# Kernel optimization log

Measured on AMD Instinct MI355X. Metric: run time of the kernel, lower is better.

The kernel has to match this reference:

```python
import jax, jax.numpy as jnp
import numpy as np

N, E = 50000, 800000
F_IN, HID, HEADS, OUT = 128, 32, 4, 16
NEG_SLOPE = 0.2  # PyG GATConv default leaky_relu slope


def segment_softmax(logits, seg, n):
    # numerically stable softmax over edges grouped by destination node
    m = jax.ops.segment_max(logits, seg, num_segments=n)          # [N,H]
    m = jnp.where(jnp.isfinite(m), m, 0.0)                        # guard empty segments
    e = jnp.exp(logits - m[seg])                                  # [E,H]
    s = jax.ops.segment_sum(e, seg, num_segments=n)               # [N,H]
    return e / (s[seg] + 1e-16)


def gat_conv(x, W, a_src, a_dst, bias, src, dst, concat):
    H, C = a_src.shape
    n = x.shape[0]
    h = (x @ W).reshape(n, H, C)                                  # [N,H,C]
    alpha_src = jnp.einsum('nhc,hc->nh', h, a_src)                # [N,H]
    alpha_dst = jnp.einsum('nhc,hc->nh', h, a_dst)                # [N,H]
    e = jax.nn.leaky_relu(alpha_src[src] + alpha_dst[dst], NEG_SLOPE)  # [E,H]
    alpha = segment_softmax(e, dst, n)                            # [E,H]
    msg = h[src] * alpha[:, :, None]                              # [E,H,C]
    out = jax.ops.segment_sum(msg, dst, num_segments=n)           # [N,H,C]
    out = out.reshape(n, H * C) if concat else out.mean(axis=1)
    return out + bias


def setup_inputs() -> dict:
    key = jax.random.key(0)
    ks = jax.random.split(key, 12)
    s = 0.1  # keep attention logits in a sane range
    return {
        'x': jax.random.normal(ks[0], (N, F_IN), jnp.float32),
        'edge_index': jax.random.randint(ks[1], (2, E), 0, N),
        'Wemb': jax.random.normal(ks[2], (F_IN, HID), jnp.float32) * s,
        'bemb': jnp.zeros((HID,), jnp.float32),
        'W1': jax.random.normal(ks[3], (HID, HEADS * HID), jnp.float32) * s,
        'a_src1': jax.random.normal(ks[4], (HEADS, HID), jnp.float32) * s,
        'a_dst1': jax.random.normal(ks[5], (HEADS, HID), jnp.float32) * s,
        'b1': jnp.zeros((HEADS * HID,), jnp.float32),
        'W2': jax.random.normal(ks[6], (HEADS * HID, HEADS * OUT), jnp.float32) * s,
        'a_src2': jax.random.normal(ks[7], (HEADS, OUT), jnp.float32) * s,
        'a_dst2': jax.random.normal(ks[8], (HEADS, OUT), jnp.float32) * s,
        'b2': jnp.zeros((OUT,), jnp.float32),
    }


def reference(x, edge_index, Wemb, bemb, W1, a_src1, a_dst1, b1, W2, a_src2, a_dst2, b2):
    src, dst = edge_index[0], edge_index[1]
    h = x @ Wemb + bemb  # dropout layers are identity at inference
    h = jax.nn.elu(gat_conv(h, W1, a_src1, a_dst1, b1, src, dst, True))
    h = gat_conv(h, W2, a_src2, a_dst2, b2, src, dst, False)
    return jax.nn.log_softmax(h, axis=1)
```

## Files before the change

### kernel.cpp

```cpp
#include <hip/hip_runtime.h>

#define N_NODES 50000
#define N_EDGES 800000
#define F_IN    128
#define HID     32
#define HEADS   4
#define OUT_C   16

#define NBKT 196
#define CAP  5120
#define EPB  4096
#define NB64 782

typedef __attribute__((ext_vector_type(8))) short bf16x8;
typedef __attribute__((ext_vector_type(4))) float f32x4;

__device__ __forceinline__ unsigned short f2bf(float f) {
    unsigned int u = __float_as_uint(f);
    u += 0x7FFFu + ((u >> 16) & 1u);
    return (unsigned short)(u >> 16);
}
__device__ __forceinline__ float bf_lo(unsigned int u) { return __uint_as_float(u << 16); }
__device__ __forceinline__ float bf_hi(unsigned int u) { return __uint_as_float(u & 0xFFFF0000u); }
__device__ __forceinline__ float bf2f(unsigned short s) {
    return __uint_as_float(((unsigned int)s) << 16);
}

__device__ __forceinline__ float edge_w(float asv, float adv) {
    float v = asv + adv;
    v = (v > 0.f) ? v : 0.2f * v;
    return __expf(v);
}

__global__ __launch_bounds__(256) void k_F1(const float* __restrict__ x,
                                            const float* __restrict__ Wemb,
                                            const float* __restrict__ bemb,
                                            float* __restrict__ h0,
                                            unsigned short* __restrict__ h0b,
                                            const int* __restrict__ ei,
                                            int* __restrict__ gcnt,
                                            unsigned int* __restrict__ pairs) {
    __shared__ float xs[64][132];
    __shared__ float Wl[F_IN][HID];
    __shared__ float bl[HID];
    __shared__ int hist[NBKT];
    __shared__ int base[NBKT];
    int t = threadIdx.x;
    if (blockIdx.x < NB64) {
        int node0 = blockIdx.x * 64;
        if (t < HID) bl[t] = bemb[t];
        #pragma unroll
        for (int it = 0; it < 4; it++) {
            int idx = it * 256 + t;
            *(float4*)((float*)Wl + idx * 4) = *(const float4*)(Wemb + idx * 4);
        }
        #pragma unroll
        for (int it = 0; it < 8; it++) {
            int idx = it * 256 + t;
            int row = idx >> 5, c4 = idx & 31;
            float4 v = make_float4(0.f, 0.f, 0.f, 0.f);
            if (node0 + row < N_NODES) v = *(const float4*)(x + (size_t)(node0 + row) * F_IN + c4 * 4);
            *(float4*)&xs[row][c4 * 4] = v;
        }
        __syncthreads();
        int c = t & 7, g = t >> 3;
        float acc[2][4] = {};
        for (int k = 0; k < F_IN; k++) {
            float4 w4 = *(const float4*)&Wl[k][c * 4];
            #pragma unroll
            for (int n = 0; n < 2; n++) {
                float xv = xs[g * 2 + n][k];
                acc[n][0] += xv * w4.x; acc[n][1] += xv * w4.y;
                acc[n][2] += xv * w4.z; acc[n][3] += xv * w4.w;
            }
        }
        #pragma unroll
        for (int n = 0; n < 2; n++) {
            int node = node0 + g * 2 + n;
            if (node < N_NODES) {
                float4 o = make_float4(acc[n][0] + bl[c * 4], acc[n][1] + bl[c * 4 + 1],
                                       acc[n][2] + bl[c * 4 + 2], acc[n][3] + bl[c * 4 + 3]);
                *(float4*)(h0 + (size_t)node * HID + c * 4) = o;
                ushort4 ob;
                ob.x = f2bf(o.x); ob.y = f2bf(o.y); ob.z = f2bf(o.z); ob.w = f2bf(o.w);
                *(ushort4*)(h0b + (size_t)node * HID + c * 4) = ob;
            }
        }
    } else {
        int e0 = (blockIdx.x - NB64) * EPB;
        for (int i = t; i < NBKT; i += 256) hist[i] = 0;
        __syncthreads();
        unsigned int p[16];
        int bb[16];
        #pragma unroll
        for (int i = 0; i < 16; i++) {
            int e = e0 + i * 256 + t;
            bb[i] = -1;
            if (e < N_EDGES) {
                int s = ei[e], d = ei[N_EDGES + e];
                p[i] = ((unsigned int)s << 8) | (unsigned int)(d & 255);
                bb[i] = d >> 8;
                atomicAdd(&hist[bb[i]], 1);
            }
        }
        __syncthreads();
        for (int i = t; i < NBKT; i += 256) {
            int c = hist[i];
            base[i] = i * CAP + (c ? atomicAdd(&gcnt[i], c) : 0);
            hist[i] = 0;
        }
        __syncthreads();
        #pragma unroll
        for (int i = 0; i < 16; i++) {
            if (bb[i] >= 0) {
                int off = atomicAdd(&hist[bb[i]], 1);
                pairs[base[bb[i]] + off] = p[i];
            }
        }
    }
}

__global__ __launch_bounds__(256) void k_F2(const float* __restrict__ h0,
                                            const float* __restrict__ W1,
                                            const float* __restrict__ a_src,
                                            const float* __restrict__ a_dst,
                                            float* __restrict__ as, float* __restrict__ ad,
                                            const unsigned int* __restrict__ pairs,
                                            const int* __restrict__ gcnt,
                                            int* __restrict__ rowptr,
                                            int* __restrict__ esrc) {
    __shared__ float xs[64][36];
    __shared__ float Wl[HID][128];
    __shared__ int cnt[256];
    __shared__ int cur[256];
    __shared__ int wsum[4];
    int t = threadIdx.x;
    if (blockIdx.x < NB64) {
        int node0 = blockIdx.x * 64;
        #pragma unroll
        for (int it = 0; it < 4; it++) {
            int idx = it * 256 + t;
            *(float4*)((float*)Wl + idx * 4) = *(const float4*)(W1 + idx * 4);
        }
        #pragma unroll
        for (int it = 0; it < 2; it++) {
            int idx = it * 256 + t;
            int row = idx >> 3, c4 = idx & 7;
            float4 v = make_float4(0.f, 0.f, 0.f, 0.f);
            if (node0 + row < N_NODES) v = *(const float4*)(h0 + (size_t)(node0 + row) * HID + c4 * 4);
            *(float4*)&xs[row][c4 * 4] = v;
        }
        __syncthreads();
        int c = t & 31, g = t >> 5;
        float acc[8][4] = {};
        for (int k = 0; k < HID; k++) {
            float4 w4 = *(const float4*)&Wl[k][c * 4];
            #pragma unroll
            for (int n = 0; n < 8; n++) {
                float xv = xs[g * 8 + n][k];
                acc[n][0] += xv * w4.x; acc[n][1] += xv * w4.y;
                acc[n][2] += xv * w4.z; acc[n][3] += xv * w4.w;
            }
        }
        float4 av = *(const float4*)(a_src + c * 4);
        float4 dv = *(const float4*)(a_dst + c * 4);
        float ps[8], pd[8];
        #pragma unroll
        for (int n = 0; n < 8; n++) {
            ps[n] = acc[n][0] * av.x + acc[n][1] * av.y + acc[n][2] * av.z + acc[n][3] * av.w;
            pd[n] = acc[n][0] * dv.x + acc[n][1] * dv.y + acc[n][2] * dv.z + acc[n][3] * dv.w;
        }
        #pragma unroll
        for (int mask = 1; mask <= 4; mask <<= 1) {
            #pragma unroll
            for (int n = 0; n < 8; n++) {
                ps[n] += __shfl_xor(ps[n], mask, 64);
                pd[n] += __shfl_xor(pd[n], mask, 64);
            }
        }
        if ((c & 7) == 0) {
            int hh = c >> 3;
            #pragma unroll
            for (int n = 0; n < 8; n++) {
                int node = node0 + g * 8 + n;
                if (node < N_NODES) { as[node * 4 + hh] = ps[n]; ad[node * 4 + hh] = pd[n]; }
            }
        }
    } else {
        int b = blockIdx.x - NB64;
        int lane = t & 63, wv = t >> 6;
        int v0 = (t < NBKT && t < b) ? gcnt[t] : 0;
        #pragma unroll
        for (int mask = 1; mask < 64; mask <<= 1) v0 += __shfl_xor(v0, mask, 64);
        if (lane == 0) wsum[wv] = v0;
        __syncthreads();
        int base = wsum[0] + wsum[1] + wsum[2] + wsum[3];
        int n0 = b << 8;
        int cntb = gcnt[b];
        int s0 = b * CAP;
        cnt[t] = 0;
        __syncthreads();
        for (int i = t; i < cntb; i += 256) atomicAdd(&cnt[pairs[s0 + i] & 255], 1);
        __syncthreads();
        int v = cnt[t], x = v;
        #pragma unroll
        for (int off = 1; off < 64; off <<= 1) { int y = __shfl_up(x, off, 64); if (lane >= off) x += y; }
        __syncthreads();
        if (lane == 63) wsum[wv] = x;
        __syncthreads();
        int add = 0;
        for (int j = 0; j < wv; j++) add += wsum[j];
        int excl = base + (x - v) + add;
        cur[t] = excl;
        if (n0 + t < N_NODES) rowptr[n0 + t] = excl;
        if (b == 0 && t == 0) rowptr[N_NODES] = N_EDGES;
        __syncthreads();
        for (int i = t; i < cntb; i += 256) {
            unsigned int p = pairs[s0 + i];
            int pos = atomicAdd(&cur[p & 255], 1);
            esrc[pos] = (int)(p >> 8);
        }
    }
}

__global__ __launch_bounds__(256) void k_h2f(const unsigned int* __restrict__ hin,
                                             const float* __restrict__ W2,
                                             const float* __restrict__ a_src,
                                             const float* __restrict__ a_dst,
                                             unsigned short* __restrict__ h2,
                                             float* __restrict__ as, float* __restrict__ ad) {
    __shared__ unsigned int xsu[64][68];
    __shared__ unsigned short w2t[64][136];
    int t = threadIdx.x;
    int node0 = blockIdx.x * 64;
    #pragma unroll
    for (int it = 0; it < 4; it++) {
        int idx = it * 256 + t;
        int row = idx >> 4, c4 = idx & 15;
        uint4 v = make_uint4(0u, 0u, 0u, 0u);
        if (node0 + row < N_NODES) v = *(const uint4*)(hin + (size_t)(node0 + row) * 64 + c4 * 4);
        *(uint4*)&xsu[row][c4 * 4] = v;
    }
    #pragma unroll
    for (int it = 0; it < 8; it++) {
        int idx = it * 256 + t;
        int k = idx >> 4, n4 = idx & 15;
        float4 w = *(const float4*)(W2 + k * 64 + n4 * 4);
        w2t[n4 * 4 + 0][k] = f2bf(w.x);
        w2t[n4 * 4 + 1][k] = f2bf(w.y);
        w2t[n4 * 4 + 2][k] = f2bf(w.z);
        w2t[n4 * 4 + 3][k] = f2bf(w.w);
    }
    __syncthreads();
    int lane = t & 63, wv = t >> 6;
    int lrow = lane & 15, lk = lane >> 4;
    f32x4 acc[4] = {};
    const char* xbase = (const char*)&xsu[wv * 16 + lrow][0] + lk * 16;
    #pragma unroll
    for (int kt = 0; kt < 4; kt++) {
        bf16x8 af = *(const bf16x8*)(xbase + kt * 64);
        #pragma unroll
        for (int h = 0; h < 4; h++) {
            bf16x8 bfr = *(const bf16x8*)((const char*)&w2t[h * 16 + lrow][0] + kt * 64 + lk * 16);
            acc[h] = __builtin_amdgcn_mfma_f32_16x16x32_bf16(af, bfr, acc[h], 0, 0, 0);
        }
    }
    float av[4], dv[4];
    #pragma unroll
    for (int h = 0; h < 4; h++) { av[h] = a_src[h * 16 + lrow]; dv[h] = a_dst[h * 16 + lrow]; }
    #pragma unroll
    for (int r = 0; r < 4; r++) {
        int node = node0 + wv * 16 + lk * 4 + r;
        float psh[4], pdh[4];
        #pragma unroll
        for (int h = 0; h < 4; h++) {
            float v = acc[h][r];
            if (node < N_NODES) h2[(size_t)node * 64 + h * 16 + lrow] = f2bf(v);
            float p = v * av[h], q = v * dv[h];
            #pragma unroll
            for (int mask = 1; mask < 16; mask <<= 1) {
                p += __shfl_xor(p, mask, 64);
                q += __shfl_xor(q, mask, 64);
            }
            psh[h] = p; pdh[h] = q;
        }
        if (lrow == 0 && node < N_NODES) {
            *(float4*)(as + node * 4) = make_float4(psh[0], psh[1], psh[2], psh[3]);
            *(float4*)(ad + node * 4) = make_float4(pdh[0], pdh[1], pdh[2], pdh[3]);
        }
    }
}

__global__ __launch_bounds__(256) void k_gather1(const int* __restrict__ esrc,
                                                 const int* __restrict__ rowptr,
                                                 const unsigned int* __restrict__ h0b,
                                                 const float* __restrict__ as,
                                                 const float* __restrict__ ad,
                                                 const float* __restrict__ W1,
                                                 const float* __restrict__ b1,
                                                 unsigned int* __restrict__ out1) {
    __shared__ float Wl[HID][128];
    __shared__ float aw[4][4][32];
    int t = threadIdx.x;
    #pragma unroll
    for (int it = 0; it < 4; it++) {
        int idx = it * 256 + t;
        *(float4*)((float*)Wl + idx * 4) = *(const float4*)(W1 + idx * 4);
    }
    int node = blockIdx.x * 4 + (t >> 6);
    int lane = t & 63;
    int head = lane >> 4;
    int cp = lane & 15;
    int s16 = lane >> 2;
    int h4 = lane & 3;
    int lb = cp * 4;
    int hb = head * 4;
    int beg = rowptr[node], end = rowptr[node + 1];
    float ad_w = ad[node * 4 + h4];
    float ax = 0.f, ay = 0.f, s = 0.f;
    const char* hc = (const char*)h0b;
    for (int k = beg; k < end; k += 16) {
        int idx = k + s16;
        int sm = esrc[min(idx, end - 1)];
#define G1L(J) int sj##J = __builtin_amdgcn_readlane(sm, (J) * 4); \
        unsigned int u##J = *(const unsigned int*)(hc + (size_t)(unsigned)sj##J * 64 + lb);
        G1L(0)  G1L(1)  G1L(2)  G1L(3)  G1L(4)  G1L(5)  G1L(6)  G1L(7)
        G1L(8)  G1L(9)  G1L(10) G1L(11) G1L(12) G1L(13) G1L(14) G1L(15)
#undef G1L
        float wm = edge_w(as[sm * 4 + h4], ad_w);
        if (idx >= end) wm = 0.f;
        int wmi = __float_as_int(wm);
#define G1W(J) float w##J = __int_as_float(__builtin_amdgcn_ds_bpermute(hb + (J) * 16, wmi));
        G1W(0)  G1W(1)  G1W(2)  G1W(3)  G1W(4)  G1W(5)  G1W(6)  G1W(7)
        G1W(8)  G1W(9)  G1W(10) G1W(11) G1W(12) G1W(13) G1W(14) G1W(15)
#undef G1W
        ax += bf_lo(u0)  * w0  + bf_lo(u1)  * w1  + bf_lo(u2)  * w2  + bf_lo(u3)  * w3
            + bf_lo(u4)  * w4  + bf_lo(u5)  * w5  + bf_lo(u6)  * w6  + bf_lo(u7)  * w7
            + bf_lo(u8)  * w8  + bf_lo(u9)  * w9  + bf_lo(u10) * w10 + bf_lo(u11) * w11
            + bf_lo(u12) * w12 + bf_lo(u13) * w13 + bf_lo(u14) * w14 + bf_lo(u15) * w15;
        ay += bf_hi(u0)  * w0  + bf_hi(u1)  * w1  + bf_hi(u2)  * w2  + bf_hi(u3)  * w3
            + bf_hi(u4)  * w4  + bf_hi(u5)  * w5  + bf_hi(u6)  * w6  + bf_hi(u7)  * w7
            + bf_hi(u8)  * w8  + bf_hi(u9)  * w9  + bf_hi(u10) * w10 + bf_hi(u11) * w11
            + bf_hi(u12) * w12 + bf_hi(u13) * w13 + bf_hi(u14) * w14 + bf_hi(u15) * w15;
        s += (w0 + w1 + w2 + w3) + (w4 + w5 + w6 + w7)
           + (w8 + w9 + w10 + w11) + (w12 + w13 + w14 + w15);
    }
    float rs = 1.0f / (s + 1e-16f);
    int wv = t >> 6;
    aw[wv][head][cp * 2]     = ax * rs;
    aw[wv][head][cp * 2 + 1] = ay * rs;
    __syncthreads();
    float2 bv = *(const float2*)(b1 + 2 * lane);
    float vx = 0.f, vy = 0.f;
    #pragma unroll
    for (int k2 = 0; k2 < HID; k2++) {
        float a = aw[wv][head][k2];
        float2 w2 = *(const float2*)&Wl[k2][2 * lane];
        vx += a * w2.x; vy += a * w2.y;
    }
    vx += bv.x; vy += bv.y;
    vx = (vx > 0.f) ? vx : (__expf(vx) - 1.0f);
    vy = (vy > 0.f) ? vy : (__expf(vy) - 1.0f);
    out1[(size_t)node * 64 + lane] = ((unsigned int)f2bf(vy) << 16) | (unsigned int)f2bf(vx);
}

__global__ __launch_bounds__(256) void k_gather2(const int* __restrict__ esrc,
                                                 const int* __restrict__ rowptr,
                                                 const unsigned short* __restrict__ h2,
                                                 const float* __restrict__ as,
                                                 const float* __restrict__ ad,
                                                 const float* __restrict__ b2,
                                                 float* __restrict__ out) {
    int t = threadIdx.x;
    int node = blockIdx.x * 4 + (t >> 6);
    int lane = t & 63;
    int head = lane >> 4, c = lane & 15;
    int s16 = lane >> 2;
    int h4 = lane & 3;
    int lb = lane * 2;
    int hb = head * 4;
    int beg = rowptr[node], end = rowptr[node + 1];
    float ad_w = ad[node * 4 + h4];
    float acc = 0.f, s = 0.f;
    const char* h2c = (const char*)h2;
    for (int k = beg; k < end; k += 16) {
        int idx = k + s16;
        int sm = esrc[min(idx, end - 1)];
#define G2L(J) int sj##J = __builtin_amdgcn_readlane(sm, (J) * 4); \
        float r##J = bf2f(*(const unsigned short*)(h2c + (size_t)(unsigned)sj##J * 128 + lb));
        G2L(0)  G2L(1)  G2L(2)  G2L(3)  G2L(4)  G2L(5)  G2L(6)  G2L(7)
        G2L(8)  G2L(9)  G2L(10) G2L(11) G2L(12) G2L(13) G2L(14) G2L(15)
#undef G2L
        float wm = edge_w(as[sm * 4 + h4], ad_w);
        if (idx >= end) wm = 0.f;
        int wmi = __float_as_int(wm);
#define G2W(J) float w##J = __int_as_float(__builtin_amdgcn_ds_bpermute(hb + (J) * 16, wmi));
        G2W(0)  G2W(1)  G2W(2)  G2W(3)  G2W(4)  G2W(5)  G2W(6)  G2W(7)
        G2W(8)  G2W(9)  G2W(10) G2W(11) G2W(12) G2W(13) G2W(14) G2W(15)
#undef G2W
        acc += r0 * w0 + r1 * w1 + r2 * w2 + r3 * w3
             + r4 * w4 + r5 * w5 + r6 * w6 + r7 * w7
             + r8 * w8 + r9 * w9 + r10 * w10 + r11 * w11
             + r12 * w12 + r13 * w13 + r14 * w14 + r15 * w15;
        s += (w0 + w1 + w2 + w3) + (w4 + w5 + w6 + w7)
           + (w8 + w9 + w10 + w11) + (w12 + w13 + w14 + w15);
    }
    float v = acc * (1.0f / (s + 1e-16f));
    v += __shfl_xor(v, 16, 64);
    v += __shfl_xor(v, 32, 64);
    v = v * 0.25f + b2[c];
    float m = v;
    #pragma unroll
    for (int mask = 1; mask < 16; mask <<= 1) m = fmaxf(m, __shfl_xor(m, mask, 64));
    float ex = __expf(v - m);
    float se = ex;
    #pragma unroll
    for (int mask = 1; mask < 16; mask <<= 1) se += __shfl_xor(se, mask, 64);
    float res = (v - m) - __logf(se);
    if (lane < 16) out[(size_t)node * 16 + lane] = res;
}

extern "C" void kernel_launch(void* const* d_in, const int* in_sizes, int n_in,
                              void* d_out, int out_size, void* d_ws, size_t ws_size,
                              hipStream_t stream) {
    const float* x      = (const float*)d_in[0];
    const int*   ei     = (const int*)d_in[1];
    const float* Wemb   = (const float*)d_in[2];
    const float* bemb   = (const float*)d_in[3];
    const float* W1     = (const float*)d_in[4];
    const float* a_src1 = (const float*)d_in[5];
    const float* a_dst1 = (const float*)d_in[6];
    const float* b1     = (const float*)d_in[7];
    const float* W2     = (const float*)d_in[8];
    const float* a_src2 = (const float*)d_in[9];
    const float* a_dst2 = (const float*)d_in[10];
    const float* b2     = (const float*)d_in[11];
    float* out = (float*)d_out;

    char* ws = (char*)d_ws;
    size_t off = 0;
    auto alloc = [&](size_t bytes) { char* p = ws + off; off += (bytes + 255) & ~size_t(255); return p; };
    unsigned short* h2b   = (unsigned short*)alloc((size_t)N_NODES * 64 * 2);
    unsigned int*   out1b = (unsigned int*)alloc((size_t)N_NODES * 64 * 4);
    float*        h0    = (float*)alloc((size_t)N_NODES * HID * 4);
    unsigned short* h0b = (unsigned short*)alloc((size_t)N_NODES * HID * 2);
    int*          esrc  = (int*)alloc((size_t)N_EDGES * 4 + 64);
    unsigned int* pairs = (unsigned int*)alloc((size_t)NBKT * CAP * 4);
    float* as     = (float*)alloc((size_t)N_NODES * 4 * 4);
    float* ad     = (float*)alloc((size_t)N_NODES * 4 * 4);
    int*   rowptr = (int*)alloc((size_t)(N_NODES + 1) * 4);
    int*   gcnt   = (int*)alloc((size_t)NBKT * 4);

    const int GB = N_NODES / 4;

    hipMemsetAsync(gcnt, 0, (size_t)NBKT * 4, stream);
    k_F1<<<NB64 + NBKT, 256, 0, stream>>>(x, Wemb, bemb, h0, h0b, ei, gcnt, pairs);
    k_F2<<<NB64 + NBKT, 256, 0, stream>>>(h0, W1, a_src1, a_dst1, as, ad,
                                          pairs, gcnt, rowptr, esrc);
    k_gather1<<<GB, 256, 0, stream>>>(esrc, rowptr, (const unsigned int*)h0b, as, ad, W1, b1, out1b);
    k_h2f<<<NB64, 256, 0, stream>>>((const unsigned int*)out1b, W2, a_src2, a_dst2, h2b, as, ad);
    k_gather2<<<GB, 256, 0, stream>>>(esrc, rowptr, h2b, as, ad, b2, out);
}
```

Measured before the change: 198.4 us.

## Move layer-1 W1 projection out of gather into MFMA kernel fused with layer-2 transform

The gather kernel now writes only the normalized attention-weighted aggregate (per-head 32-wide, bf16) instead of applying W1, bias and ELU per node with scalar FMAs and an LDS copy of W1. A new kernel does the W1 projection via bf16 MFMA, applies bias+ELU into LDS, then immediately runs the W2 projection and attention-logit computation. This removes the per-block W1 load and scalar matmul from the latency-bound gather and uses tensor cores instead. In exchange it adds bf16 rounding of the aggregate and the layer-1 output, and a heavier LDS footprint in the fused kernel.

After: 192.3 us. 1.03x faster.

```diff
diff --git a/kernel.cpp b/kernel.cpp
--- a/kernel.cpp
+++ b/kernel.cpp
@@ -223,90 +223,13 @@
     }
 }
 
-__global__ __launch_bounds__(256) void k_h2f(const unsigned int* __restrict__ hin,
-                                             const float* __restrict__ W2,
-                                             const float* __restrict__ a_src,
-                                             const float* __restrict__ a_dst,
-                                             unsigned short* __restrict__ h2,
-                                             float* __restrict__ as, float* __restrict__ ad) {
-    __shared__ unsigned int xsu[64][68];
-    __shared__ unsigned short w2t[64][136];
-    int t = threadIdx.x;
-    int node0 = blockIdx.x * 64;
-    #pragma unroll
-    for (int it = 0; it < 4; it++) {
-        int idx = it * 256 + t;
-        int row = idx >> 4, c4 = idx & 15;
-        uint4 v = make_uint4(0u, 0u, 0u, 0u);
-        if (node0 + row < N_NODES) v = *(const uint4*)(hin + (size_t)(node0 + row) * 64 + c4 * 4);
-        *(uint4*)&xsu[row][c4 * 4] = v;
-    }
-    #pragma unroll
-    for (int it = 0; it < 8; it++) {
-        int idx = it * 256 + t;
-        int k = idx >> 4, n4 = idx & 15;
-        float4 w = *(const float4*)(W2 + k * 64 + n4 * 4);
-        w2t[n4 * 4 + 0][k] = f2bf(w.x);
-        w2t[n4 * 4 + 1][k] = f2bf(w.y);
-        w2t[n4 * 4 + 2][k] = f2bf(w.z);
-        w2t[n4 * 4 + 3][k] = f2bf(w.w);
-    }
-    __syncthreads();
-    int lane = t & 63, wv = t >> 6;
-    int lrow = lane & 15, lk = lane >> 4;
-    f32x4 acc[4] = {};
-    const char* xbase = (const char*)&xsu[wv * 16 + lrow][0] + lk * 16;
-    #pragma unroll
-    for (int kt = 0; kt < 4; kt++) {
-        bf16x8 af = *(const bf16x8*)(xbase + kt * 64);
-        #pragma unroll
-        for (int h = 0; h < 4; h++) {
-            bf16x8 bfr = *(const bf16x8*)((const char*)&w2t[h * 16 + lrow][0] + kt * 64 + lk * 16);
-            acc[h] = __builtin_amdgcn_mfma_f32_16x16x32_bf16(af, bfr, acc[h], 0, 0, 0);
-        }
-    }
-    float av[4], dv[4];
-    #pragma unroll
-    for (int h = 0; h < 4; h++) { av[h] = a_src[h * 16 + lrow]; dv[h] = a_dst[h * 16 + lrow]; }
-    #pragma unroll
-    for (int r = 0; r < 4; r++) {
-        int node = node0 + wv * 16 + lk * 4 + r;
-        float psh[4], pdh[4];
-        #pragma unroll
-        for (int h = 0; h < 4; h++) {
-            float v = acc[h][r];
-            if (node < N_NODES) h2[(size_t)node * 64 + h * 16 + lrow] = f2bf(v);
-            float p = v * av[h], q = v * dv[h];
-            #pragma unroll
-            for (int mask = 1; mask < 16; mask <<= 1) {
-                p += __shfl_xor(p, mask, 64);
-                q += __shfl_xor(q, mask, 64);
-            }
-            psh[h] = p; pdh[h] = q;
-        }
-        if (lrow == 0 && node < N_NODES) {
-            *(float4*)(as + node * 4) = make_float4(psh[0], psh[1], psh[2], psh[3]);
-            *(float4*)(ad + node * 4) = make_float4(pdh[0], pdh[1], pdh[2], pdh[3]);
-        }
-    }
-}
-
 __global__ __launch_bounds__(256) void k_gather1(const int* __restrict__ esrc,
                                                  const int* __restrict__ rowptr,
                                                  const unsigned int* __restrict__ h0b,
                                                  const float* __restrict__ as,
                                                  const float* __restrict__ ad,
-                                                 const float* __restrict__ W1,
-                                                 const float* __restrict__ b1,
-                                                 unsigned int* __restrict__ out1) {
-    __shared__ float Wl[HID][128];
-    __shared__ float aw[4][4][32];
+                                                 unsigned int* __restrict__ awb) {
     int t = threadIdx.x;
-    #pragma unroll
-    for (int it = 0; it < 4; it++) {
-        int idx = it * 256 + t;
-        *(float4*)((float*)Wl + idx * 4) = *(const float4*)(W1 + idx * 4);
-    }
     int node = blockIdx.x * 4 + (t >> 6);
     int lane = t & 63;
     int head = lane >> 4;
@@ -346,22 +269,110 @@
            + (w8 + w9 + w10 + w11) + (w12 + w13 + w14 + w15);
     }
     float rs = 1.0f / (s + 1e-16f);
-    int wv = t >> 6;
-    aw[wv][head][cp * 2]     = ax * rs;
-    aw[wv][head][cp * 2 + 1] = ay * rs;
+    awb[(size_t)node * 64 + lane] = ((unsigned int)f2bf(ay * rs) << 16) | (unsigned int)f2bf(ax * rs);
+}
+
+__global__ __launch_bounds__(256) void k_h12(const unsigned int* __restrict__ awb,
+                                             const float* __restrict__ W1,
+                                             const float* __restrict__ b1,
+                                             const float* __restrict__ W2,
+                                             const float* __restrict__ a_src,
+                                             const float* __restrict__ a_dst,
+                                             unsigned short* __restrict__ h2,
+                                             float* __restrict__ as, float* __restrict__ ad) {
+    __shared__ unsigned int xsu[64][68];
+    __shared__ unsigned short w1t[128][40];
+    __shared__ unsigned short w2t[64][136];
+    __shared__ float b1s[128];
+    int t = threadIdx.x;
+    int node0 = blockIdx.x * 64;
+    if (t < 128) b1s[t] = b1[t];
+    #pragma unroll
+    for (int it = 0; it < 4; it++) {
+        int idx = it * 256 + t;
+        int row = idx >> 4, c4 = idx & 15;
+        uint4 v = make_uint4(0u, 0u, 0u, 0u);
+        if (node0 + row < N_NODES) v = *(const uint4*)(awb + (size_t)(node0 + row) * 64 + c4 * 4);
+        *(uint4*)&xsu[row][c4 * 4] = v;
+    }
+    #pragma unroll
+    for (int it = 0; it < 16; it++) {
+        int idx = it * 256 + t;
+        int k = idx >> 7, n = idx & 127;
+        w1t[n][k] = f2bf(W1[idx]);
+    }
+    #pragma unroll
+    for (int it = 0; it < 8; it++) {
+        int idx = it * 256 + t;
+        int k = idx >> 4, n4 = idx & 15;
+        float4 w = *(const float4*)(W2 + k * 64 + n4 * 4);
+        w2t[n4 * 4 + 0][k] = f2bf(w.x);
+        w2t[n4 * 4 + 1][k] = f2bf(w.y);
+        w2t[n4 * 4 + 2][k] = f2bf(w.z);
+        w2t[n4 * 4 + 3][k] = f2bf(w.w);
+    }
     __syncthreads();
-    float2 bv = *(const float2*)(b1 + 2 * lane);
-    float vx = 0.f, vy = 0.f;
-    #pragma unroll
-    for (int k2 = 0; k2 < HID; k2++) {
-        float a = aw[wv][head][k2];
-        float2 w2 = *(const float2*)&Wl[k2][2 * lane];
-        vx += a * w2.x; vy += a * w2.y;
-    }
-    vx += bv.x; vy += bv.y;
-    vx = (vx > 0.f) ? vx : (__expf(vx) - 1.0f);
-    vy = (vy > 0.f) ? vy : (__expf(vy) - 1.0f);
-    out1[(size_t)node * 64 + lane] = ((unsigned int)f2bf(vy) << 16) | (unsigned int)f2bf(vx);
+    int lane = t & 63, wv = t >> 6;
+    int lrow = lane & 15, lk = lane >> 4;
+    const char* abase = (const char*)&xsu[wv * 16 + lrow][0];
+    f32x4 o1[8];
+    #pragma unroll
+    for (int nt = 0; nt < 8; nt++) {
+        int kt = nt >> 1;
+        bf16x8 af = *(const bf16x8*)(abase + kt * 64 + lk * 16);
+        bf16x8 bf1 = *(const bf16x8*)((const char*)&w1t[nt * 16 + lrow][0] + lk * 16);
+        f32x4 z = {};
+        o1[nt] = __builtin_amdgcn_mfma_f32_16x16x32_bf16(af, bf1, z, 0, 0, 0);
+    }
+    __syncthreads();
+    unsigned short* o1t = (unsigned short*)&xsu[0][0];
+    #pragma unroll
+    for (int nt = 0; nt < 8; nt++) {
+        float bb = b1s[nt * 16 + lrow];
+        #pragma unroll
+        for (int r = 0; r < 4; r++) {
+            int noderow = wv * 16 + lk * 4 + r;
+            float v = o1[nt][r] + bb;
+            v = (v > 0.f) ? v : (__expf(v) - 1.0f);
+            o1t[noderow * 136 + nt * 16 + lrow] = f2bf(v);
+        }
+    }
+    __syncthreads();
+    f32x4 acc[4] = {};
+    const char* xbase = (const char*)&o1t[(wv * 16 + lrow) * 136];
+    #pragma unroll
+    for (int kt = 0; kt < 4; kt++) {
+        bf16x8 af = *(const bf16x8*)(xbase + kt * 64 + lk * 16);
+        #pragma unroll
+        for (int h = 0; h < 4; h++) {
+            bf16x8 bfr = *(const bf16x8*)((const char*)&w2t[h * 16 + lrow][0] + kt * 64 + lk * 16);
+            acc[h] = __builtin_amdgcn_mfma_f32_16x16x32_bf16(af, bfr, acc[h], 0, 0, 0);
+        }
+    }
+    float av[4], dv[4];
+    #pragma unroll
+    for (int h = 0; h < 4; h++) { av[h] = a_src[h * 16 + lrow]; dv[h] = a_dst[h * 16 + lrow]; }
+    #pragma unroll
+    for (int r = 0; r < 4; r++) {
+        int node = node0 + wv * 16 + lk * 4 + r;
+        float psh[4], pdh[4];
+        #pragma unroll
+        for (int h = 0; h < 4; h++) {
+            float v = acc[h][r];
+            if (node < N_NODES) h2[(size_t)node * 64 + h * 16 + lrow] = f2bf(v);
+            float p = v * av[h], q = v * dv[h];
+            #pragma unroll
+            for (int mask = 1; mask < 16; mask <<= 1) {
+                p += __shfl_xor(p, mask, 64);
+                q += __shfl_xor(q, mask, 64);
+            }
+            psh[h] = p; pdh[h] = q;
+        }
+        if (lrow == 0 && node < N_NODES) {
+            *(float4*)(as + node * 4) = make_float4(psh[0], psh[1], psh[2], psh[3]);
+            *(float4*)(ad + node * 4) = make_float4(pdh[0], pdh[1], pdh[2], pdh[3]);
+        }
+    }
 }
 
 __global__ __launch_bounds__(256) void k_gather2(const int* __restrict__ esrc,
@@ -441,7 +452,7 @@
     size_t off = 0;
     auto alloc = [&](size_t bytes) { char* p = ws + off; off += (bytes + 255) & ~size_t(255); return p; };
     unsigned short* h2b   = (unsigned short*)alloc((size_t)N_NODES * 64 * 2);
-    unsigned int*   out1b = (unsigned int*)alloc((size_t)N_NODES * 64 * 4);
+    unsigned int*   awb   = (unsigned int*)alloc((size_t)N_NODES * 64 * 4);
     float*        h0    = (float*)alloc((size_t)N_NODES * HID * 4);
     unsigned short* h0b = (unsigned short*)alloc((size_t)N_NODES * HID * 2);
     int*          esrc  = (int*)alloc((size_t)N_EDGES * 4 + 64);
@@ -457,7 +468,7 @@
     k_F1<<<NB64 + NBKT, 256, 0, stream>>>(x, Wemb, bemb, h0, h0b, ei, gcnt, pairs);
     k_F2<<<NB64 + NBKT, 256, 0, stream>>>(h0, W1, a_src1, a_dst1, as, ad,
                                           pairs, gcnt, rowptr, esrc);
-    k_gather1<<<GB, 256, 0, stream>>>(esrc, rowptr, (const unsigned int*)h0b, as, ad, W1, b1, out1b);
-    k_h2f<<<NB64, 256, 0, stream>>>((const unsigned int*)out1b, W2, a_src2, a_dst2, h2b, as, ad);
+    k_gather1<<<GB, 256, 0, stream>>>(esrc, rowptr, (const unsigned int*)h0b, as, ad, awb);
+    k_h12<<<NB64, 256, 0, stream>>>(awb, W1, b1, W2, a_src2, a_dst2, h2b, as, ad);
     k_gather2<<<GB, 256, 0, stream>>>(esrc, rowptr, h2b, as, ad, b2, out);
 }
```
